# Kernel tuning notes

Hardware: AMD Instinct MI355X
Metric: run time of the kernel (lower is better)

The kernel has to match this reference:

```python
import jax, jax.numpy as jnp
import numpy as np

N, E, D, H, O = 100000, 1600000, 128, 128, 64
EPS = 1e-5


def setup_inputs() -> dict:
    key = jax.random.key(0)
    ks = jax.random.split(key, 12)
    s = 0.05
    return {
        "x": jax.random.normal(ks[0], (N, D), jnp.float32),
        "edge_index": jax.random.randint(ks[1], (2, E), 0, N),
        "W1": jax.random.normal(ks[2], (D, H), jnp.float32) * s,
        "b1": jnp.zeros((H,), jnp.float32),
        "W2": jax.random.normal(ks[3], (H, H), jnp.float32) * s,
        "b2": jnp.zeros((H,), jnp.float32),
        "W3": jax.random.normal(ks[4], (H, H), jnp.float32) * s,
        "b3": jnp.zeros((H,), jnp.float32),
        "g1": jnp.ones((H,), jnp.float32),
        "be1": jnp.zeros((H,), jnp.float32),
        "g2": jnp.ones((H,), jnp.float32),
        "be2": jnp.zeros((H,), jnp.float32),
        "Wp1": jax.random.normal(ks[5], (H, H), jnp.float32) * s,
        "bp1": jnp.zeros((H,), jnp.float32),
        "Wp2": jax.random.normal(ks[6], (H, O), jnp.float32) * s,
        "bp2": jnp.zeros((O,), jnp.float32),
    }


def _layer_norm(h, g, b):
    mu = jnp.mean(h, axis=-1, keepdims=True)
    var = jnp.mean(jnp.square(h - mu), axis=-1, keepdims=True)
    return g * (h - mu) * jax.lax.rsqrt(var + EPS) + b


def reference(x, edge_index, W1, b1, W2, b2, W3, b3, g1, be1, g2, be2, Wp1, bp1, Wp2, bp2):
    n = x.shape[0]
    loop = jnp.arange(n)
    # GCN: add self-loops, symmetric normalization D^-1/2 (A+I) D^-1/2
    src = jnp.concatenate([edge_index[0], loop])
    dst = jnp.concatenate([edge_index[1], loop])
    deg = jax.ops.segment_sum(jnp.ones_like(src, x.dtype), dst, num_segments=n)
    dinv = jax.lax.rsqrt(jnp.maximum(deg, 1e-12))
    norm = dinv[src] * dinv[dst]  # [E+N]

    def gcn_conv(h, W, b):
        hw = h @ W                              # transform first (PyG GCNConv)
        msg = hw[src] * norm[:, None]           # gather + edge scale
        return jax.ops.segment_sum(msg, dst, num_segments=n) + b  # scatter-add

    # dropout is a no-op in eval mode
    h = _layer_norm(jax.nn.relu(gcn_conv(x, W1, b1)), g1, be1)
    h = _layer_norm(jax.nn.relu(gcn_conv(h, W2, b2)), g2, be2)
    h = jax.nn.relu(gcn_conv(h, W3, b3))
    h = h @ Wp1 + bp1
    h = h @ Wp2 + bp2
    return jax.nn.sigmoid(h)
```

## Files before the change

kernel.cpp:

```cpp
#include <hip/hip_runtime.h>
#include <hip/hip_bf16.h>

typedef __attribute__((ext_vector_type(8))) short short8;
typedef __attribute__((ext_vector_type(4))) float floatx4;
typedef unsigned int u32;

__device__ __forceinline__ float bf2f(u32 u) {
    union { u32 u; float f; } c; c.u = u << 16; return c.f;
}
__device__ __forceinline__ float bf2f_hi(u32 u) {
    union { u32 u; float f; } c; c.u = u & 0xFFFF0000u; return c.f;
}
__device__ __forceinline__ u32 f2bf(float f) {
    union { float f; u32 u; } c; c.f = f;
    return (c.u + 0x7FFFu + ((c.u >> 16) & 1u)) >> 16;
}
__device__ __forceinline__ short8 cvt8(const float* p) {
    float4 f0 = ((const float4*)p)[0];
    float4 f1 = ((const float4*)p)[1];
    short8 r;
    r[0] = (short)f2bf(f0.x); r[1] = (short)f2bf(f0.y);
    r[2] = (short)f2bf(f0.z); r[3] = (short)f2bf(f0.w);
    r[4] = (short)f2bf(f1.x); r[5] = (short)f2bf(f1.y);
    r[6] = (short)f2bf(f1.z); r[7] = (short)f2bf(f1.w);
    return r;
}

__device__ __forceinline__ void fp8x2_acc(u32 v, float& a0, float& a1) {
    auto f = __builtin_amdgcn_cvt_pk_f32_fp8((int)v, false);
    a0 += ((const float*)&f)[0];
    a1 += ((const float*)&f)[1];
}
__device__ __forceinline__ void fp8x2_dec(u32 v, float& x, float& y) {
    auto f = __builtin_amdgcn_cvt_pk_f32_fp8((int)v, false);
    x = ((const float*)&f)[0];
    y = ((const float*)&f)[1];
}
__device__ __forceinline__ u32 f32x4_to_fp8(float a, float b, float c, float d) {
    u32 w = (u32)__builtin_amdgcn_cvt_pk_fp8_f32(a, b, 0, false);
    w = (u32)__builtin_amdgcn_cvt_pk_fp8_f32(c, d, (int)w, true);
    return w;
}

__device__ __forceinline__ void gather4(const unsigned short* __restrict__ hw,
                                        const int* __restrict__ col,
                                        int beg, int e1, int e2, int e3, int e4,
                                        int lane, float* __restrict__ A0,
                                        float* __restrict__ A1) {
    float c0 = 0.f, c1 = 0.f;
    int seg = 0, segend = e1;
#define FLUSH_SEG() do { \
        if (seg == 0)      { A0[0] = c0; A1[0] = c1; segend = e2; } \
        else if (seg == 1) { A0[1] = c0; A1[1] = c1; segend = e3; } \
        else if (seg == 2) { A0[2] = c0; A1[2] = c1; segend = e4; } \
        else               { A0[3] = c0; A1[3] = c1; segend = 0x7fffffff; } \
        c0 = 0.f; c1 = 0.f; ++seg; } while (0)

    int idx0 = beg + lane;
    int svc = (idx0 < e4) ? col[idx0] : 0;
    for (int c = beg; c < e4; c += 64) {
        int idxn = c + 64 + lane;
        int svn = (idxn < e4) ? col[idxn] : 0;
        int m = e4 - c; if (m > 64) m = 64;
        int e = 0;
        for (; e + 32 <= m; e += 32) {
            u32 v[32];
#pragma unroll
            for (int j = 0; j < 32; ++j) {
                int s = __builtin_amdgcn_readlane(svc, e + j);
                v[j] = hw[(size_t)s * 64 + lane];
            }
            int gb = c + e;
            if (gb + 31 < segend) {
#pragma unroll
                for (int j = 0; j < 32; ++j) fp8x2_acc(v[j], c0, c1);
            } else {
#pragma unroll
                for (int j = 0; j < 32; ++j) {
                    while (gb + j >= segend) FLUSH_SEG();
                    fp8x2_acc(v[j], c0, c1);
                }
            }
        }
        for (; e + 8 <= m; e += 8) {
            u32 v[8];
#pragma unroll
            for (int j = 0; j < 8; ++j) {
                int s = __builtin_amdgcn_readlane(svc, e + j);
                v[j] = hw[(size_t)s * 64 + lane];
            }
            int gb = c + e;
            if (gb + 7 < segend) {
#pragma unroll
                for (int j = 0; j < 8; ++j) fp8x2_acc(v[j], c0, c1);
            } else {
#pragma unroll
                for (int j = 0; j < 8; ++j) {
                    while (gb + j >= segend) FLUSH_SEG();
                    fp8x2_acc(v[j], c0, c1);
                }
            }
        }
        for (; e < m; ++e) {
            int s = __builtin_amdgcn_readlane(svc, e);
            u32 v = hw[(size_t)s * 64 + lane];
            while (c + e >= segend) FLUSH_SEG();
            fp8x2_acc(v, c0, c1);
        }
        svc = svn;
    }
    while (seg < 4) FLUSH_SEG();
#undef FLUSH_SEG
}

__global__ __launch_bounds__(256) void hist_trans_k(
        const int* __restrict__ dst, int* __restrict__ bcnt, int E, int histB,
        const float* __restrict__ W1, const float* __restrict__ W2,
        const float* __restrict__ W3, const float* __restrict__ Wp1,
        const float* __restrict__ Wp2,
        unsigned short* __restrict__ o1, unsigned short* __restrict__ o2,
        unsigned short* __restrict__ o3, unsigned short* __restrict__ o4,
        unsigned short* __restrict__ o5) {
    int t = threadIdx.x;
    if ((int)blockIdx.x < histB) {
        __shared__ int h[512];
        h[t] = 0; h[t + 256] = 0;
        __syncthreads();
        int e0 = blockIdx.x * 4096;
        int ne = min(4096, E - e0);
        for (int i = t; i < ne; i += 256) atomicAdd(&h[dst[e0 + i] >> 8], 1);
        __syncthreads();
        int c = h[t];
        if (c) atomicAdd(&bcnt[t], c);
        c = h[t + 256];
        if (c) atomicAdd(&bcnt[t + 256], c);
    } else {
        int i = (blockIdx.x - histB) * 256 + t;
        const float* in; unsigned short* out; int cols, li;
        if (i < 16384)      { in = W1;  out = o1; cols = 128; li = i; }
        else if (i < 32768) { in = W2;  out = o2; cols = 128; li = i - 16384; }
        else if (i < 49152) { in = W3;  out = o3; cols = 128; li = i - 32768; }
        else if (i < 65536) { in = Wp1; out = o4; cols = 128; li = i - 49152; }
        else                { in = Wp2; out = o5; cols = 64;  li = i - 65536; }
        int r = li / cols, c = li - r * cols;
        out[(size_t)c * 128 + r] = (unsigned short)f2bf(in[li]);
    }
}

__global__ void bscan_k(const int* __restrict__ bcnt, int* __restrict__ bbase,
                        int* __restrict__ cursor, int nb, int E) {
    __shared__ int tmp[512];
    int t = threadIdx.x;
    int v = (t < nb) ? bcnt[t] : 0;
    tmp[t] = v;
    __syncthreads();
    for (int off = 1; off < 512; off <<= 1) {
        int a = (t >= off) ? tmp[t - off] : 0;
        __syncthreads();
        tmp[t] += a;
        __syncthreads();
    }
    if (t < nb) {
        int ex = tmp[t] - v;
        bbase[t] = ex;
        cursor[t] = ex;
    }
    if (t == 0) bbase[nb] = E;
}

__global__ __launch_bounds__(256) void bucket_k(const int* __restrict__ src,
                                                const int* __restrict__ dst,
                                                int* __restrict__ cursor,
                                                u32* __restrict__ pairs, int E, int nb) {
    __shared__ int cnt[512];
    __shared__ int gbase[512];
    __shared__ int cur[512];
    int t = threadIdx.x;
    cnt[t] = 0; cnt[t + 256] = 0;
    __syncthreads();
    int e0 = blockIdx.x * 8192;
    int ne = min(8192, E - e0);
    for (int i = t; i < ne; i += 256) atomicAdd(&cnt[dst[e0 + i] >> 8], 1);
    __syncthreads();
    for (int b = t; b < nb; b += 256) {
        int c = cnt[b];
        gbase[b] = c ? atomicAdd(&cursor[b], c) : 0;
        cur[b] = 0;
    }
    __syncthreads();
    for (int i = t; i < ne; i += 256) {
        int d = dst[e0 + i];
        int s = src[e0 + i];
        int b = d >> 8;
        int p = atomicAdd(&cur[b], 1);
        pairs[gbase[b] + p] = (u32)s | ((u32)(d & 255) << 24);
    }
}

#define LCOL_CAP 12288
__global__ __launch_bounds__(256) void build_k(const u32* __restrict__ pairs,
                                               const int* __restrict__ bbase,
                                               int* __restrict__ rowptr,
                                               float* __restrict__ dinv,
                                               int* __restrict__ col, int N, int E) {
    __shared__ int cnt[256], incl[256], cur[256];
    __shared__ int lcol[LCOL_CAP];
    int b = blockIdx.x, t = threadIdx.x;
    int base = bbase[b];
    int ecnt = bbase[b + 1] - base;
    cnt[t] = 0;
    __syncthreads();
    for (int j = t; j < ecnt; j += 256) atomicAdd(&cnt[pairs[base + j] >> 24], 1);
    __syncthreads();
    incl[t] = cnt[t];
    __syncthreads();
    for (int off = 1; off < 256; off <<= 1) {
        int a = (t >= off) ? incl[t - off] : 0;
        __syncthreads();
        incl[t] += a;
        __syncthreads();
    }
    int myc = cnt[t];
    int ex = incl[t] - myc;
    int node = b * 256 + t;
    if (node < N) {
        rowptr[node] = base + ex;
        dinv[node] = rsqrtf((float)myc + 1.0f);
    }
    cur[t] = ex;
    if (b == 0 && t == 0) rowptr[N] = E;
    __syncthreads();
    if (ecnt <= LCOL_CAP) {
        for (int j = t; j < ecnt; j += 256) {
            u32 v = pairs[base + j];
            int r = atomicAdd(&cur[v >> 24], 1);
            lcol[r] = (int)(v & 0xFFFFFF);
        }
        __syncthreads();
        for (int j = t; j < ecnt; j += 256) col[base + j] = lcol[j];
    } else {
        for (int j = t; j < ecnt; j += 256) {
            u32 v = pairs[base + j];
            int r = atomicAdd(&cur[v >> 24], 1);
            col[base + r] = (int)(v & 0xFFFFFF);
        }
    }
}

__global__ __launch_bounds__(256) void gemm1_k(const float* __restrict__ A,
                                               const short* __restrict__ Wt,
                                               const float* __restrict__ dinv,
                                               u32* __restrict__ out, int M) {
    int wave = threadIdx.x >> 6;
    int lane = threadIdx.x & 63;
    int m0 = blockIdx.x * 64 + wave * 16;
    if (m0 >= M) return;
    int quad = lane >> 4, lr = lane & 15;
    int row = m0 + lr;
    bool wr = row < M;
    if (row >= M) row = M - 1;
    const float* Ab = A + (size_t)row * 128 + quad * 8;
    short8 b0 = cvt8(Ab), b1 = cvt8(Ab + 32), b2 = cvt8(Ab + 64), b3 = cvt8(Ab + 96);
    float di = dinv[row];
#pragma unroll
    for (int nt = 0; nt < 8; ++nt) {
        int ncol = nt * 16 + lr;
        const short8* Wp = (const short8*)(Wt + (size_t)ncol * 128 + quad * 8);
        short8 a0 = Wp[0], a1 = Wp[4], a2 = Wp[8], a3 = Wp[12];
        floatx4 acc = {0.f, 0.f, 0.f, 0.f};
        acc = __builtin_amdgcn_mfma_f32_16x16x32_bf16(a0, b0, acc, 0, 0, 0);
        acc = __builtin_amdgcn_mfma_f32_16x16x32_bf16(a1, b1, acc, 0, 0, 0);
        acc = __builtin_amdgcn_mfma_f32_16x16x32_bf16(a2, b2, acc, 0, 0, 0);
        acc = __builtin_amdgcn_mfma_f32_16x16x32_bf16(a3, b3, acc, 0, 0, 0);
        if (wr) {
            out[(size_t)(m0 + lr) * 32 + nt * 4 + quad] =
                f32x4_to_fp8(acc[0] * di, acc[1] * di, acc[2] * di, acc[3] * di);
        }
    }
}

__global__ __launch_bounds__(256) void fconv_k(const unsigned short* __restrict__ hw,
                                               const int* __restrict__ rowptr,
                                               const int* __restrict__ col,
                                               const float* __restrict__ dinv,
                                               const float* __restrict__ bias,
                                               const float* __restrict__ gam,
                                               const float* __restrict__ bet,
                                               const short* __restrict__ Wt,
                                               u32* __restrict__ out, int N) {
    __shared__ unsigned short rows[16][136];
    int t = threadIdx.x, wave = t >> 6, lane = t & 63;
    int nb0 = blockIdx.x * 16;
    int node0 = nb0 + wave * 4;
    int ridx = node0 + (lane < 4 ? lane : 4);
    if (ridx > N) ridx = N;
    int rp = rowptr[ridx];
    int beg = __builtin_amdgcn_readlane(rp, 0);
    int e1  = __builtin_amdgcn_readlane(rp, 1);
    int e2  = __builtin_amdgcn_readlane(rp, 2);
    int e3  = __builtin_amdgcn_readlane(rp, 3);
    int e4  = __builtin_amdgcn_readlane(rp, 4);
    u32 selfv[4]; float dv[4];
#pragma unroll
    for (int i = 0; i < 4; ++i) {
        int node = node0 + i;
        bool ok = node < N;
        selfv[i] = ok ? (u32)hw[(size_t)node * 64 + lane] : 0u;
        dv[i]    = ok ? dinv[node] : 0.f;
    }
    float A0[4], A1[4];
    gather4(hw, col, beg, e1, e2, e3, e4, lane, A0, A1);
#pragma unroll
    for (int i = 0; i < 4; ++i) {
        int r = wave * 4 + i;
        int node = node0 + i;
        float a0 = 0.f, a1 = 0.f;
        if (node < N) {
            float di = dv[i];
            float sx, sy;
            fp8x2_dec(selfv[i], sx, sy);
            a0 = di * (A0[i] + sx);
            a1 = di * (A1[i] + sy);
            a0 = fmaxf(a0 + bias[2 * lane], 0.f);
            a1 = fmaxf(a1 + bias[2 * lane + 1], 0.f);
            float s = a0 + a1, q = a0 * a0 + a1 * a1;
#pragma unroll
            for (int m = 32; m >= 1; m >>= 1) {
                s += __shfl_xor(s, m, 64);
                q += __shfl_xor(q, m, 64);
            }
            float mu = s * (1.f / 128.f);
            float var = q * (1.f / 128.f) - mu * mu;
            float rs = rsqrtf(fmaxf(var, 0.f) + 1e-5f);
            a0 = gam[2 * lane] * (a0 - mu) * rs + bet[2 * lane];
            a1 = gam[2 * lane + 1] * (a1 - mu) * rs + bet[2 * lane + 1];
        }
        ((u32*)&rows[r][0])[lane] = f2bf(a0) | (f2bf(a1) << 16);
    }
    __syncthreads();
    int quad = lane >> 4, lr = lane & 15;
    short8 b0 = *(const short8*)&rows[lr][quad * 8];
    short8 b1 = *(const short8*)&rows[lr][32 + quad * 8];
    short8 b2 = *(const short8*)&rows[lr][64 + quad * 8];
    short8 b3 = *(const short8*)&rows[lr][96 + quad * 8];
    int onode = nb0 + lr;
    float di2 = (onode < N) ? dinv[onode] : 0.f;
#pragma unroll
    for (int k = 0; k < 2; ++k) {
        int ct = wave * 2 + k;
        int ncol = ct * 16 + lr;
        const short8* Wp = (const short8*)(Wt + (size_t)ncol * 128 + quad * 8);
        short8 a0 = Wp[0], a1 = Wp[4], a2 = Wp[8], a3 = Wp[12];
        floatx4 acc = {0.f, 0.f, 0.f, 0.f};
        acc = __builtin_amdgcn_mfma_f32_16x16x32_bf16(a0, b0, acc, 0, 0, 0);
        acc = __builtin_amdgcn_mfma_f32_16x16x32_bf16(a1, b1, acc, 0, 0, 0);
        acc = __builtin_amdgcn_mfma_f32_16x16x32_bf16(a2, b2, acc, 0, 0, 0);
        acc = __builtin_amdgcn_mfma_f32_16x16x32_bf16(a3, b3, acc, 0, 0, 0);
        int c0 = ct * 16 + quad * 4;
        if (onode < N) {
            out[(size_t)onode * 32 + (c0 >> 2)] =
                f32x4_to_fp8(acc[0] * di2, acc[1] * di2, acc[2] * di2, acc[3] * di2);
        }
    }
}

__global__ __launch_bounds__(256) void fhead_k(const unsigned short* __restrict__ hw,
                                               const int* __restrict__ rowptr,
                                               const int* __restrict__ col,
                                               const float* __restrict__ dinv,
                                               const float* __restrict__ bias,
                                               const short* __restrict__ Wp1t,
                                               const float* __restrict__ bp1,
                                               const short* __restrict__ Wp2t,
                                               const float* __restrict__ bp2,
                                               float* __restrict__ out, int N) {
    __shared__ unsigned short rows[16][136];
    __shared__ unsigned short h1s[16][136];
    int t = threadIdx.x, wave = t >> 6, lane = t & 63;
    int nb0 = blockIdx.x * 16;
    int node0 = nb0 + wave * 4;
    int ridx = node0 + (lane < 4 ? lane : 4);
    if (ridx > N) ridx = N;
    int rp = rowptr[ridx];
    int beg = __builtin_amdgcn_readlane(rp, 0);
    int e1  = __builtin_amdgcn_readlane(rp, 1);
    int e2  = __builtin_amdgcn_readlane(rp, 2);
    int e3  = __builtin_amdgcn_readlane(rp, 3);
    int e4  = __builtin_amdgcn_readlane(rp, 4);
    u32 selfv[4]; float dv[4];
#pragma unroll
    for (int i = 0; i < 4; ++i) {
        int node = node0 + i;
        bool ok = node < N;
        selfv[i] = ok ? (u32)hw[(size_t)node * 64 + lane] : 0u;
        dv[i]    = ok ? dinv[node] : 0.f;
    }
    float A0[4], A1[4];
    gather4(hw, col, beg, e1, e2, e3, e4, lane, A0, A1);
#pragma unroll
    for (int i = 0; i < 4; ++i) {
        int r = wave * 4 + i;
        int node = node0 + i;
        float a0 = 0.f, a1 = 0.f;
        if (node < N) {
            float di = dv[i];
            float sx, sy;
            fp8x2_dec(selfv[i], sx, sy);
            a0 = di * (A0[i] + sx);
            a1 = di * (A1[i] + sy);
            a0 = fmaxf(a0 + bias[2 * lane], 0.f);
            a1 = fmaxf(a1 + bias[2 * lane + 1], 0.f);
        }
        ((u32*)&rows[r][0])[lane] = f2bf(a0) | (f2bf(a1) << 16);
    }
    __syncthreads();
    int quad = lane >> 4, lr = lane & 15;
    {
        short8 b0 = *(const short8*)&rows[lr][quad * 8];
        short8 b1 = *(const short8*)&rows[lr][32 + quad * 8];
        short8 b2 = *(const short8*)&rows[lr][64 + quad * 8];
        short8 b3 = *(const short8*)&rows[lr][96 + quad * 8];
#pragma unroll
        for (int k = 0; k < 2; ++k) {
            int ct = wave * 2 + k;
            int ncol = ct * 16 + lr;
            const short8* Wp = (const short8*)(Wp1t + (size_t)ncol * 128 + quad * 8);
            short8 a0 = Wp[0], a1 = Wp[4], a2 = Wp[8], a3 = Wp[12];
            floatx4 acc = {0.f, 0.f, 0.f, 0.f};
            acc = __builtin_amdgcn_mfma_f32_16x16x32_bf16(a0, b0, acc, 0, 0, 0);
            acc = __builtin_amdgcn_mfma_f32_16x16x32_bf16(a1, b1, acc, 0, 0, 0);
            acc = __builtin_amdgcn_mfma_f32_16x16x32_bf16(a2, b2, acc, 0, 0, 0);
            acc = __builtin_amdgcn_mfma_f32_16x16x32_bf16(a3, b3, acc, 0, 0, 0);
            int c0 = ct * 16 + quad * 4;
            float4 bv = *(const float4*)(bp1 + c0);
            uint2 st;
            st.x = f2bf(acc[0] + bv.x) | (f2bf(acc[1] + bv.y) << 16);
            st.y = f2bf(acc[2] + bv.z) | (f2bf(acc[3] + bv.w) << 16);
            *(uint2*)&h1s[lr][c0] = st;
        }
    }
    __syncthreads();
    {
        short8 b0 = *(const short8*)&h1s[lr][quad * 8];
        short8 b1 = *(const short8*)&h1s[lr][32 + quad * 8];
        short8 b2 = *(const short8*)&h1s[lr][64 + quad * 8];
        short8 b3 = *(const short8*)&h1s[lr][96 + quad * 8];
        int ncol = wave * 16 + lr;
        const short8* Wp = (const short8*)(Wp2t + (size_t)ncol * 128 + quad * 8);
        short8 a0 = Wp[0], a1 = Wp[4], a2 = Wp[8], a3 = Wp[12];
        floatx4 acc = {0.f, 0.f, 0.f, 0.f};
        acc = __builtin_amdgcn_mfma_f32_16x16x32_bf16(a0, b0, acc, 0, 0, 0);
        acc = __builtin_amdgcn_mfma_f32_16x16x32_bf16(a1, b1, acc, 0, 0, 0);
        acc = __builtin_amdgcn_mfma_f32_16x16x32_bf16(a2, b2, acc, 0, 0, 0);
        acc = __builtin_amdgcn_mfma_f32_16x16x32_bf16(a3, b3, acc, 0, 0, 0);
        int c0 = wave * 16 + quad * 4;
        int onode = nb0 + lr;
        if (onode < N) {
            float4 bv = *(const float4*)(bp2 + c0);
            float4 st;
            st.x = 1.f / (1.f + __expf(-(acc[0] + bv.x)));
            st.y = 1.f / (1.f + __expf(-(acc[1] + bv.y)));
            st.z = 1.f / (1.f + __expf(-(acc[2] + bv.z)));
            st.w = 1.f / (1.f + __expf(-(acc[3] + bv.w)));
            *(float4*)(out + (size_t)onode * 64 + c0) = st;
        }
    }
}

extern "C" void kernel_launch(void* const* d_in, const int* in_sizes, int n_in,
                              void* d_out, int out_size, void* d_ws, size_t ws_size,
                              hipStream_t stream) {
    const int N = in_sizes[0] / 128;
    const int E = in_sizes[1] / 2;
    const int nb = (N + 255) >> 8;
    const int* edge = (const int*)d_in[1];
    const int* srcp = edge;
    const int* dstp = edge + E;
    const float* x   = (const float*)d_in[0];
    const float* W1  = (const float*)d_in[2];
    const float* b1  = (const float*)d_in[3];
    const float* W2  = (const float*)d_in[4];
    const float* b2  = (const float*)d_in[5];
    const float* W3  = (const float*)d_in[6];
    const float* b3  = (const float*)d_in[7];
    const float* g1  = (const float*)d_in[8];
    const float* be1 = (const float*)d_in[9];
    const float* g2  = (const float*)d_in[10];
    const float* be2 = (const float*)d_in[11];
    const float* Wp1 = (const float*)d_in[12];
    const float* bp1 = (const float*)d_in[13];
    const float* Wp2 = (const float*)d_in[14];
    const float* bp2 = (const float*)d_in[15];

    char* ws = (char*)d_ws;
    size_t off = 0;
    auto alloc = [&](size_t b) -> char* {
        char* p = ws + off;
        off += (b + 255) & ~(size_t)255;
        return p;
    };
    int* bcnt   = (int*)alloc(512 * 4);
    int* bbase  = (int*)alloc((size_t)(nb + 1) * 4);
    int* cursor = (int*)alloc((size_t)nb * 4);
    int* rowptr = (int*)alloc((size_t)(N + 1) * 4);
    float* dinv = (float*)alloc((size_t)N * 4);
    u32* pairs  = (u32*)alloc((size_t)E * 4);
    int* colA   = (int*)alloc((size_t)E * 4);
    unsigned char* hw  = (unsigned char*)alloc((size_t)N * 128);
    unsigned char* hb  = (unsigned char*)alloc((size_t)N * 128);
    unsigned short* w1t = (unsigned short*)alloc(128 * 128 * 2);
    unsigned short* w2t = (unsigned short*)alloc(128 * 128 * 2);
    unsigned short* w3t = (unsigned short*)alloc(128 * 128 * 2);
    unsigned short* wp1t = (unsigned short*)alloc(128 * 128 * 2);
    unsigned short* wp2t = (unsigned short*)alloc(64 * 128 * 2);
    if (off > ws_size) return;

    int gb = (N + 63) / 64;
    int fb = (N + 15) / 16;
    int histB = (E + 4095) / 4096;

    hipMemsetAsync(bcnt, 0, 512 * 4, stream);
    hist_trans_k<<<histB + 288, 256, 0, stream>>>(dstp, bcnt, E, histB,
                                                  W1, W2, W3, Wp1, Wp2,
                                                  w1t, w2t, w3t, wp1t, wp2t);
    bscan_k<<<1, 512, 0, stream>>>(bcnt, bbase, cursor, nb, E);
    bucket_k<<<(E + 8191) / 8192, 256, 0, stream>>>(srcp, dstp, cursor, pairs, E, nb);
    build_k<<<nb, 256, 0, stream>>>(pairs, bbase, rowptr, dinv, colA, N, E);

    gemm1_k<<<gb, 256, 0, stream>>>(x, (const short*)w1t, dinv, (u32*)hw, N);
    fconv_k<<<fb, 256, 0, stream>>>((const unsigned short*)hw, rowptr, colA, dinv,
                                    b1, g1, be1, (const short*)w2t, (u32*)hb, N);
    fconv_k<<<fb, 256, 0, stream>>>((const unsigned short*)hb, rowptr, colA, dinv,
                                    b2, g2, be2, (const short*)w3t, (u32*)hw, N);
    fhead_k<<<fb, 256, 0, stream>>>((const unsigned short*)hw, rowptr, colA, dinv, b3,
                                    (const short*)wp1t, bp1, (const short*)wp2t, bp2,
                                    (float*)d_out, N);
}
```

Baseline: 406.9 us.

## Gather two neighbor rows per wave using half-wave dword loads of fp8 features

The fp8 neighbor gather now has each half-wave load one 128-byte row as 32 dwords, so a wave fetches two edges per load instruction instead of one row via 16-bit loads per lane. Partial sums from the two halves are combined with a cross-half shuffle when a segment is flushed. Segment boundaries that fall between the two edges of a pair need a slow path. The LayerNorm reduction shrinks to 32 lanes and bias, gamma and beta are loaded as float4. The aim is fewer memory instructions and better use of the gather bandwidth, at the cost of extra shuffles and more complex boundary handling.

```diff
diff --git a/kernel.cpp b/kernel.cpp
--- a/kernel.cpp
+++ b/kernel.cpp
@@ -5,12 +5,6 @@
 typedef __attribute__((ext_vector_type(4))) float floatx4;
 typedef unsigned int u32;
 
-__device__ __forceinline__ float bf2f(u32 u) {
-    union { u32 u; float f; } c; c.u = u << 16; return c.f;
-}
-__device__ __forceinline__ float bf2f_hi(u32 u) {
-    union { u32 u; float f; } c; c.u = u & 0xFFFF0000u; return c.f;
-}
 __device__ __forceinline__ u32 f2bf(float f) {
     union { float f; u32 u; } c; c.f = f;
     return (c.u + 0x7FFFu + ((c.u >> 16) & 1u)) >> 16;
@@ -26,15 +20,21 @@
     return r;
 }
 
-__device__ __forceinline__ void fp8x2_acc(u32 v, float& a0, float& a1) {
-    auto f = __builtin_amdgcn_cvt_pk_f32_fp8((int)v, false);
-    a0 += ((const float*)&f)[0];
-    a1 += ((const float*)&f)[1];
-}
-__device__ __forceinline__ void fp8x2_dec(u32 v, float& x, float& y) {
-    auto f = __builtin_amdgcn_cvt_pk_f32_fp8((int)v, false);
-    x = ((const float*)&f)[0];
-    y = ((const float*)&f)[1];
+__device__ __forceinline__ void fp8x4_acc(u32 v, float& c0, float& c1, float& c2, float& c3) {
+    auto flo = __builtin_amdgcn_cvt_pk_f32_fp8((int)v, false);
+    auto fhi = __builtin_amdgcn_cvt_pk_f32_fp8((int)v, true);
+    c0 += ((const float*)&flo)[0];
+    c1 += ((const float*)&flo)[1];
+    c2 += ((const float*)&fhi)[0];
+    c3 += ((const float*)&fhi)[1];
+}
+__device__ __forceinline__ void fp8x4_dec(u32 v, float& x0, float& x1, float& x2, float& x3) {
+    auto flo = __builtin_amdgcn_cvt_pk_f32_fp8((int)v, false);
+    auto fhi = __builtin_amdgcn_cvt_pk_f32_fp8((int)v, true);
+    x0 = ((const float*)&flo)[0];
+    x1 = ((const float*)&flo)[1];
+    x2 = ((const float*)&fhi)[0];
+    x3 = ((const float*)&fhi)[1];
 }
 __device__ __forceinline__ u32 f32x4_to_fp8(float a, float b, float c, float d) {
     u32 w = (u32)__builtin_amdgcn_cvt_pk_fp8_f32(a, b, 0, false);
@@ -42,19 +42,35 @@
     return w;
 }
 
-__device__ __forceinline__ void gather4(const unsigned short* __restrict__ hw,
-                                        const int* __restrict__ col,
-                                        int beg, int e1, int e2, int e3, int e4,
-                                        int lane, float* __restrict__ A0,
-                                        float* __restrict__ A1) {
-    float c0 = 0.f, c1 = 0.f;
+__device__ __forceinline__ void gather4p(const u32* __restrict__ hw32,
+                                         const int* __restrict__ col,
+                                         int beg, int e1, int e2, int e3, int e4,
+                                         int lane,
+                                         float* __restrict__ A0, float* __restrict__ A1,
+                                         float* __restrict__ A2, float* __restrict__ A3) {
+    float c0 = 0.f, c1 = 0.f, c2 = 0.f, c3 = 0.f;
     int seg = 0, segend = e1;
+    int l32 = lane & 31;
+    bool lo_half = lane < 32;
 #define FLUSH_SEG() do { \
-        if (seg == 0)      { A0[0] = c0; A1[0] = c1; segend = e2; } \
-        else if (seg == 1) { A0[1] = c0; A1[1] = c1; segend = e3; } \
-        else if (seg == 2) { A0[2] = c0; A1[2] = c1; segend = e4; } \
-        else               { A0[3] = c0; A1[3] = c1; segend = 0x7fffffff; } \
-        c0 = 0.f; c1 = 0.f; ++seg; } while (0)
+        c0 += __shfl_xor(c0, 32); c1 += __shfl_xor(c1, 32); \
+        c2 += __shfl_xor(c2, 32); c3 += __shfl_xor(c3, 32); \
+        if (seg == 0)      { A0[0]=c0; A1[0]=c1; A2[0]=c2; A3[0]=c3; segend = e2; } \
+        else if (seg == 1) { A0[1]=c0; A1[1]=c1; A2[1]=c2; A3[1]=c3; segend = e3; } \
+        else if (seg == 2) { A0[2]=c0; A1[2]=c1; A2[2]=c2; A3[2]=c3; segend = e4; } \
+        else if (seg == 3) { A0[3]=c0; A1[3]=c1; A2[3]=c2; A3[3]=c3; segend = 0x7fffffff; } \
+        c0=c1=c2=c3=0.f; ++seg; } while (0)
+
+#define PAIR_SLOW(vv, gb) do { \
+        while ((gb) >= segend) FLUSH_SEG(); \
+        if ((gb) + 1 < segend) { \
+            fp8x4_acc((vv), c0, c1, c2, c3); \
+        } else { \
+            if (lo_half) fp8x4_acc((vv), c0, c1, c2, c3); \
+            FLUSH_SEG(); \
+            while ((gb) + 1 >= segend) FLUSH_SEG(); \
+            if (!lo_half) fp8x4_acc((vv), c0, c1, c2, c3); \
+        } } while (0)
 
     int idx0 = beg + lane;
     int svc = (idx0 < e4) ? col[idx0] : 0;
@@ -62,54 +78,57 @@
         int idxn = c + 64 + lane;
         int svn = (idxn < e4) ? col[idxn] : 0;
         int m = e4 - c; if (m > 64) m = 64;
-        int e = 0;
-        for (; e + 32 <= m; e += 32) {
-            u32 v[32];
-#pragma unroll
-            for (int j = 0; j < 32; ++j) {
-                int s = __builtin_amdgcn_readlane(svc, e + j);
-                v[j] = hw[(size_t)s * 64 + lane];
+        int np = (m + 1) >> 1;
+        int pb = 0;
+        for (; pb + 16 <= np; pb += 16) {
+            u32 v[16];
+#pragma unroll
+            for (int j = 0; j < 16; ++j) {
+                int jj = pb + j;
+                int slo = __builtin_amdgcn_readlane(svc, 2 * jj);
+                int shi = __builtin_amdgcn_readlane(svc, 2 * jj + 1);
+                int r = lo_half ? slo : shi;
+                v[j] = hw32[(size_t)r * 32 + l32];
             }
-            int gb = c + e;
-            if (gb + 31 < segend) {
-#pragma unroll
-                for (int j = 0; j < 32; ++j) fp8x2_acc(v[j], c0, c1);
+            int gb0 = c + 2 * pb;
+            if (gb0 + 31 < segend) {
+#pragma unroll
+                for (int j = 0; j < 16; ++j) fp8x4_acc(v[j], c0, c1, c2, c3);
             } else {
 #pragma unroll
-                for (int j = 0; j < 32; ++j) {
-                    while (gb + j >= segend) FLUSH_SEG();
-                    fp8x2_acc(v[j], c0, c1);
-                }
+                for (int j = 0; j < 16; ++j) PAIR_SLOW(v[j], gb0 + 2 * j);
             }
         }
-        for (; e + 8 <= m; e += 8) {
-            u32 v[8];
-#pragma unroll
-            for (int j = 0; j < 8; ++j) {
-                int s = __builtin_amdgcn_readlane(svc, e + j);
-                v[j] = hw[(size_t)s * 64 + lane];
+        for (; pb + 4 <= np; pb += 4) {
+            u32 v[4];
+#pragma unroll
+            for (int j = 0; j < 4; ++j) {
+                int jj = pb + j;
+                int slo = __builtin_amdgcn_readlane(svc, 2 * jj);
+                int shi = __builtin_amdgcn_readlane(svc, 2 * jj + 1);
+                int r = lo_half ? slo : shi;
+                v[j] = hw32[(size_t)r * 32 + l32];
             }
-            int gb = c + e;
-            if (gb + 7 < segend) {
-#pragma unroll
-                for (int j = 0; j < 8; ++j) fp8x2_acc(v[j], c0, c1);
+            int gb0 = c + 2 * pb;
+            if (gb0 + 7 < segend) {
+#pragma unroll
+                for (int j = 0; j < 4; ++j) fp8x4_acc(v[j], c0, c1, c2, c3);
             } else {
 #pragma unroll
-                for (int j = 0; j < 8; ++j) {
-                    while (gb + j >= segend) FLUSH_SEG();
-                    fp8x2_acc(v[j], c0, c1);
-                }
+                for (int j = 0; j < 4; ++j) PAIR_SLOW(v[j], gb0 + 2 * j);
             }
         }
-        for (; e < m; ++e) {
-            int s = __builtin_amdgcn_readlane(svc, e);
-            u32 v = hw[(size_t)s * 64 + lane];
-            while (c + e >= segend) FLUSH_SEG();
-            fp8x2_acc(v, c0, c1);
+        for (; pb < np; ++pb) {
+            int slo = __builtin_amdgcn_readlane(svc, 2 * pb);
+            int shi = __builtin_amdgcn_readlane(svc, 2 * pb + 1);
+            int r = lo_half ? slo : shi;
+            u32 v = hw32[(size_t)r * 32 + l32];
+            PAIR_SLOW(v, c + 2 * pb);
         }
         svc = svn;
     }
     while (seg < 4) FLUSH_SEG();
+#undef PAIR_SLOW
 #undef FLUSH_SEG
 }
 
@@ -279,7 +298,7 @@
     }
 }
 
-__global__ __launch_bounds__(256) void fconv_k(const unsigned short* __restrict__ hw,
+__global__ __launch_bounds__(256) void fconv_k(const u32* __restrict__ hw32,
                                                const int* __restrict__ rowptr,
                                                const int* __restrict__ col,
                                                const float* __restrict__ dinv,
@@ -290,6 +309,7 @@
                                                u32* __restrict__ out, int N) {
     __shared__ unsigned short rows[16][136];
     int t = threadIdx.x, wave = t >> 6, lane = t & 63;
+    int l32 = lane & 31;
     int nb0 = blockIdx.x * 16;
     int node0 = nb0 + wave * 4;
     int ridx = node0 + (lane < 4 ? lane : 4);
@@ -300,42 +320,57 @@
     int e2  = __builtin_amdgcn_readlane(rp, 2);
     int e3  = __builtin_amdgcn_readlane(rp, 3);
     int e4  = __builtin_amdgcn_readlane(rp, 4);
-    u32 selfv[4]; float dv[4];
+    u32 selfd[4]; float dv[4];
 #pragma unroll
     for (int i = 0; i < 4; ++i) {
         int node = node0 + i;
         bool ok = node < N;
-        selfv[i] = ok ? (u32)hw[(size_t)node * 64 + lane] : 0u;
+        selfd[i] = ok ? hw32[(size_t)node * 32 + l32] : 0u;
         dv[i]    = ok ? dinv[node] : 0.f;
     }
-    float A0[4], A1[4];
-    gather4(hw, col, beg, e1, e2, e3, e4, lane, A0, A1);
+    float A0[4], A1[4], A2[4], A3[4];
+    gather4p(hw32, col, beg, e1, e2, e3, e4, lane, A0, A1, A2, A3);
 #pragma unroll
     for (int i = 0; i < 4; ++i) {
         int r = wave * 4 + i;
         int node = node0 + i;
-        float a0 = 0.f, a1 = 0.f;
+        float a0 = 0.f, a1 = 0.f, a2 = 0.f, a3 = 0.f;
         if (node < N) {
             float di = dv[i];
-            float sx, sy;
-            fp8x2_dec(selfv[i], sx, sy);
-            a0 = di * (A0[i] + sx);
-            a1 = di * (A1[i] + sy);
-            a0 = fmaxf(a0 + bias[2 * lane], 0.f);
-            a1 = fmaxf(a1 + bias[2 * lane + 1], 0.f);
-            float s = a0 + a1, q = a0 * a0 + a1 * a1;
-#pragma unroll
-            for (int m = 32; m >= 1; m >>= 1) {
-                s += __shfl_xor(s, m, 64);
-                q += __shfl_xor(q, m, 64);
+            float s0, s1, s2, s3;
+            fp8x4_dec(selfd[i], s0, s1, s2, s3);
+            a0 = di * (A0[i] + s0);
+            a1 = di * (A1[i] + s1);
+            a2 = di * (A2[i] + s2);
+            a3 = di * (A3[i] + s3);
+            float4 bv = *(const float4*)(bias + 4 * l32);
+            a0 = fmaxf(a0 + bv.x, 0.f);
+            a1 = fmaxf(a1 + bv.y, 0.f);
+            a2 = fmaxf(a2 + bv.z, 0.f);
+            a3 = fmaxf(a3 + bv.w, 0.f);
+            float s = a0 + a1 + a2 + a3;
+            float q = a0 * a0 + a1 * a1 + a2 * a2 + a3 * a3;
+#pragma unroll
+            for (int mm = 16; mm >= 1; mm >>= 1) {
+                s += __shfl_xor(s, mm);
+                q += __shfl_xor(q, mm);
             }
             float mu = s * (1.f / 128.f);
             float var = q * (1.f / 128.f) - mu * mu;
             float rs = rsqrtf(fmaxf(var, 0.f) + 1e-5f);
-            a0 = gam[2 * lane] * (a0 - mu) * rs + bet[2 * lane];
-            a1 = gam[2 * lane + 1] * (a1 - mu) * rs + bet[2 * lane + 1];
-        }
-        ((u32*)&rows[r][0])[lane] = f2bf(a0) | (f2bf(a1) << 16);
+            float4 gv = *(const float4*)(gam + 4 * l32);
+            float4 bev = *(const float4*)(bet + 4 * l32);
+            a0 = gv.x * (a0 - mu) * rs + bev.x;
+            a1 = gv.y * (a1 - mu) * rs + bev.y;
+            a2 = gv.z * (a2 - mu) * rs + bev.z;
+            a3 = gv.w * (a3 - mu) * rs + bev.w;
+        }
+        if (lane < 32) {
+            uint2 st;
+            st.x = f2bf(a0) | (f2bf(a1) << 16);
+            st.y = f2bf(a2) | (f2bf(a3) << 16);
+            *(uint2*)&rows[r][4 * l32] = st;
+        }
     }
     __syncthreads();
     int quad = lane >> 4, lr = lane & 15;
@@ -364,7 +399,7 @@
     }
 }
 
-__global__ __launch_bounds__(256) void fhead_k(const unsigned short* __restrict__ hw,
+__global__ __launch_bounds__(256) void fhead_k(const u32* __restrict__ hw32,
                                                const int* __restrict__ rowptr,
                                                const int* __restrict__ col,
                                                const float* __restrict__ dinv,
@@ -377,6 +412,7 @@
     __shared__ unsigned short rows[16][136];
     __shared__ unsigned short h1s[16][136];
     int t = threadIdx.x, wave = t >> 6, lane = t & 63;
+    int l32 = lane & 31;
     int nb0 = blockIdx.x * 16;
     int node0 = nb0 + wave * 4;
     int ridx = node0 + (lane < 4 ? lane : 4);
@@ -387,31 +423,41 @@
     int e2  = __builtin_amdgcn_readlane(rp, 2);
     int e3  = __builtin_amdgcn_readlane(rp, 3);
     int e4  = __builtin_amdgcn_readlane(rp, 4);
-    u32 selfv[4]; float dv[4];
+    u32 selfd[4]; float dv[4];
 #pragma unroll
     for (int i = 0; i < 4; ++i) {
         int node = node0 + i;
         bool ok = node < N;
-        selfv[i] = ok ? (u32)hw[(size_t)node * 64 + lane] : 0u;
+        selfd[i] = ok ? hw32[(size_t)node * 32 + l32] : 0u;
         dv[i]    = ok ? dinv[node] : 0.f;
     }
-    float A0[4], A1[4];
-    gather4(hw, col, beg, e1, e2, e3, e4, lane, A0, A1);
+    float A0[4], A1[4], A2[4], A3[4];
+    gather4p(hw32, col, beg, e1, e2, e3, e4, lane, A0, A1, A2, A3);
 #pragma unroll
     for (int i = 0; i < 4; ++i) {
         int r = wave * 4 + i;
         int node = node0 + i;
-        float a0 = 0.f, a1 = 0.f;
+        float a0 = 0.f, a1 = 0.f, a2 = 0.f, a3 = 0.f;
         if (node < N) {
             float di = dv[i];
-            float sx, sy;
-            fp8x2_dec(selfv[i], sx, sy);
-            a0 = di * (A0[i] + sx);
-            a1 = di * (A1[i] + sy);
-            a0 = fmaxf(a0 + bias[2 * lane], 0.f);
-            a1 = fmaxf(a1 + bias[2 * lane + 1], 0.f);
-        }
-        ((u32*)&rows[r][0])[lane] = f2bf(a0) | (f2bf(a1) << 16);
+            float s0, s1, s2, s3;
+            fp8x4_dec(selfd[i], s0, s1, s2, s3);
+            a0 = di * (A0[i] + s0);
+            a1 = di * (A1[i] + s1);
+            a2 = di * (A2[i] + s2);
+            a3 = di * (A3[i] + s3);
+            float4 bv = *(const float4*)(bias + 4 * l32);
+            a0 = fmaxf(a0 + bv.x, 0.f);
+            a1 = fmaxf(a1 + bv.y, 0.f);
+            a2 = fmaxf(a2 + bv.z, 0.f);
+            a3 = fmaxf(a3 + bv.w, 0.f);
+        }
+        if (lane < 32) {
+            uint2 st;
+            st.x = f2bf(a0) | (f2bf(a1) << 16);
+            st.y = f2bf(a2) | (f2bf(a3) << 16);
+            *(uint2*)&rows[r][4 * l32] = st;
+        }
     }
     __syncthreads();
     int quad = lane >> 4, lr = lane & 15;
@@ -528,11 +574,11 @@
     build_k<<<nb, 256, 0, stream>>>(pairs, bbase, rowptr, dinv, colA, N, E);
 
     gemm1_k<<<gb, 256, 0, stream>>>(x, (const short*)w1t, dinv, (u32*)hw, N);
-    fconv_k<<<fb, 256, 0, stream>>>((const unsigned short*)hw, rowptr, colA, dinv,
+    fconv_k<<<fb, 256, 0, stream>>>((const u32*)hw, rowptr, colA, dinv,
                                     b1, g1, be1, (const short*)w2t, (u32*)hb, N);
-    fconv_k<<<fb, 256, 0, stream>>>((const unsigned short*)hb, rowptr, colA, dinv,
+    fconv_k<<<fb, 256, 0, stream>>>((const u32*)hb, rowptr, colA, dinv,
                                     b2, g2, be2, (const short*)w3t, (u32*)hw, N);
-    fhead_k<<<fb, 256, 0, stream>>>((const unsigned short*)hw, rowptr, colA, dinv, b3,
+    fhead_k<<<fb, 256, 0, stream>>>((const u32*)hw, rowptr, colA, dinv, b3,
                                     (const short*)wp1t, bp1, (const short*)wp2t, bp2,
                                     (float*)d_out, N);
 }
```

Measured after the change: 460.4 us. +13.2%, slower.
